# Optimization experiments

Measured on AMD Instinct MI355X. Metric: run time of the kernel, lower is better.

## Reference

```python
import jax, jax.numpy as jnp
import numpy as np

N = 100000      # nodes
E = 1600000     # edges
IN_DIM = 500
HID = 64
OUT = 40
BN_EPS = 1e-5


def setup_inputs() -> dict:
    key = jax.random.key(0)
    ks = jax.random.split(key, 20)
    x = jax.random.normal(ks[0], (N, IN_DIM), dtype=jnp.float32)
    edge_index = jax.random.randint(ks[1], (2, E), 0, N, dtype=jnp.int64)

    def lin(k, fin, fout):
        return jax.random.normal(k, (fin, fout), dtype=jnp.float32) / np.sqrt(fin).astype(np.float32)

    inp = {
        "x": x,
        "edge_index": edge_index,
        "W1": lin(ks[2], IN_DIM, HID),
        "b1": jnp.zeros((HID,), jnp.float32),
        "g1": jnp.ones((HID,), jnp.float32),
        "be1": jnp.zeros((HID,), jnp.float32),
        "m1": 0.1 * jax.random.normal(ks[3], (HID,), jnp.float32),
        "v1": jax.random.uniform(ks[4], (HID,), jnp.float32, 0.5, 1.5),
        "W2": lin(ks[5], HID, HID),
        "b2": jnp.zeros((HID,), jnp.float32),
        "g2": jnp.ones((HID,), jnp.float32),
        "be2": jnp.zeros((HID,), jnp.float32),
        "m2": 0.1 * jax.random.normal(ks[6], (HID,), jnp.float32),
        "v2": jax.random.uniform(ks[7], (HID,), jnp.float32, 0.5, 1.5),
        "W3": lin(ks[8], HID, OUT),
        "b3": jnp.zeros((OUT,), jnp.float32),
    }
    return inp


def _gcn_conv(h, src, dst, deg_inv_sqrt, W, b):
    # PyG GCNConv (add_self_loops=True, normalize=True, eval math):
    # out = D^-1/2 (A + I) D^-1/2 (h @ W) + b
    h = h @ W                                    # [N, F]
    norm = deg_inv_sqrt[src] * deg_inv_sqrt[dst]  # [E]
    msg = h[src] * norm[:, None]                  # [E, F] gather
    agg = jax.ops.segment_sum(msg, dst, num_segments=N)  # scatter-add
    agg = agg + h * (deg_inv_sqrt * deg_inv_sqrt)[:, None]  # self-loop term
    return agg + b


def reference(x, edge_index, W1, b1, g1, be1, m1, v1,
              W2, b2, g2, be2, m2, v2, W3, b3):
    src, dst = edge_index[0], edge_index[1]
    # degree including self-loop
    deg = jax.ops.segment_sum(jnp.ones((E,), x.dtype), dst, num_segments=N) + 1.0
    deg_inv_sqrt = jax.lax.rsqrt(deg)

    def bn(h, g, be, m, v):
        return (h - m) * jax.lax.rsqrt(v + BN_EPS) * g + be

    h = _gcn_conv(x, src, dst, deg_inv_sqrt, W1, b1)
    h = jax.nn.relu(bn(h, g1, be1, m1, v1))
    # dropout: identity in eval mode
    h = _gcn_conv(h, src, dst, deg_inv_sqrt, W2, b2)
    h = jax.nn.relu(bn(h, g2, be2, m2, v2))
    out = _gcn_conv(h, src, dst, deg_inv_sqrt, W3, b3)
    return jax.nn.log_softmax(out, axis=1)
```

## Files before the change

### kernel.cpp

```cpp
#include <hip/hip_runtime.h>
#include <math.h>

#define N_NODES 100000
#define N_EDGES 1600000
#define IN_DIM  500
#define HID     64
#define OUT_DIM 40
#define BN_EPS  1e-5f
#define SCAN_NB 98
#define NTILE   6250

typedef _Float16 f16;
typedef __attribute__((ext_vector_type(2))) _Float16 f16x2;
typedef __attribute__((ext_vector_type(8))) _Float16 f16x8;
typedef __attribute__((ext_vector_type(4))) float f32x4;

static inline int cdiv(long a, int b) { return (int)((a + b - 1) / b); }

__device__ inline unsigned short f2h_bits(float f) {
    f16 h = (f16)f;
    return __builtin_bit_cast(unsigned short, h);
}
__device__ inline f16x2 bits2h2(unsigned int u) {
    return __builtin_bit_cast(f16x2, u);
}

__global__ void k_count_deg(const int* __restrict__ ei, int* degi) {
    int e = blockIdx.x * 256 + threadIdx.x;
    if (e < N_EDGES) atomicAdd(&degi[ei[N_EDGES + e]], 1);
}

__global__ void k_scan1(const int* __restrict__ degi, int* __restrict__ rowptr,
                        int* __restrict__ blocksum, float* __restrict__ dis) {
    __shared__ int sd[256];
    int tid = threadIdx.x;
    int base = blockIdx.x * 1024 + tid * 4;
    int v0 = (base + 0 < N_NODES) ? degi[base + 0] : 0;
    int v1 = (base + 1 < N_NODES) ? degi[base + 1] : 0;
    int v2 = (base + 2 < N_NODES) ? degi[base + 2] : 0;
    int v3 = (base + 3 < N_NODES) ? degi[base + 3] : 0;
    if (base + 0 < N_NODES) dis[base + 0] = rsqrtf((float)v0 + 1.0f);
    if (base + 1 < N_NODES) dis[base + 1] = rsqrtf((float)v1 + 1.0f);
    if (base + 2 < N_NODES) dis[base + 2] = rsqrtf((float)v2 + 1.0f);
    if (base + 3 < N_NODES) dis[base + 3] = rsqrtf((float)v3 + 1.0f);
    int s = v0 + v1 + v2 + v3;
    sd[tid] = s;
    __syncthreads();
    for (int off = 1; off < 256; off <<= 1) {
        int t = (tid >= off) ? sd[tid - off] : 0;
        __syncthreads();
        sd[tid] += t;
        __syncthreads();
    }
    int excl = sd[tid] - s;
    if (base + 0 < N_NODES) rowptr[base + 0] = excl;
    if (base + 1 < N_NODES) rowptr[base + 1] = excl + v0;
    if (base + 2 < N_NODES) rowptr[base + 2] = excl + v0 + v1;
    if (base + 3 < N_NODES) rowptr[base + 3] = excl + v0 + v1 + v2;
    if (tid == 255) blocksum[blockIdx.x] = sd[255];
}

__global__ void k_scan2(int* __restrict__ blocksum, int* __restrict__ blockbase) {
    __shared__ int sd[128];
    int tid = threadIdx.x;
    int v = (tid < SCAN_NB) ? blocksum[tid] : 0;
    sd[tid] = v;
    __syncthreads();
    for (int off = 1; off < 128; off <<= 1) {
        int t = (tid >= off) ? sd[tid - off] : 0;
        __syncthreads();
        sd[tid] += t;
        __syncthreads();
    }
    if (tid < SCAN_NB) blockbase[tid] = sd[tid] - v;
}

__global__ void k_scan3(int* __restrict__ rowptr, const int* __restrict__ blockbase) {
    int add = blockbase[blockIdx.x];
    int base = blockIdx.x * 1024 + threadIdx.x * 4;
#pragma unroll
    for (int i = 0; i < 4; ++i)
        if (base + i < N_NODES) rowptr[base + i] += add;
}

__global__ void k_permute(const int* __restrict__ ei, const int* __restrict__ rowptr,
                          int* __restrict__ cursor, const float* __restrict__ dis,
                          uint2* __restrict__ epack) {
    int e = blockIdx.x * 256 + threadIdx.x;
    if (e >= N_EDGES) return;
    int s = ei[e];
    int d = ei[N_EDGES + e];
    int pos = rowptr[d] + atomicAdd(&cursor[d], 1);
    unsigned int hb = f2h_bits(dis[s] * dis[d]);
    epack[pos] = make_uint2((unsigned int)(s * 128), (hb << 16) | hb);
}

__device__ inline void convW_one(const float* W, unsigned short* wb,
                                 int idx, int K, int F) {
    int j    = idx & 7;
    int lane = (idx >> 3) & 63;
    int q    = idx >> 9;
    int t    = q >> 2, nt = q & 3;
    int n = nt * 16 + (lane & 15);
    int k = t * 32 + ((lane >> 4) << 3) + j;
    float v = (k < K && n < F) ? W[(long)k * F + n] : 0.f;
    wb[idx] = f2h_bits(v);
}

__global__ void k_convall(const float* __restrict__ W1, const float* __restrict__ W2,
                          const float* __restrict__ W3,
                          unsigned short* __restrict__ wb1,
                          unsigned short* __restrict__ wb2,
                          unsigned short* __restrict__ wb3) {
    int idx = blockIdx.x * 256 + threadIdx.x;
    if (idx < 32768) {
        convW_one(W1, wb1, idx, IN_DIM, HID);
    } else if (idx < 36864) {
        convW_one(W2, wb2, idx - 32768, HID, HID);
    } else {
        convW_one(W3, wb3, idx - 36864, HID, OUT_DIM);
    }
}

__global__ __launch_bounds__(256) void k_l1fused(
        const float* __restrict__ x,
        const unsigned short* __restrict__ wb,
        unsigned short* __restrict__ h) {
    __shared__ unsigned short l[16 * 520];
    const int rt = blockIdx.x;
    const int tid = threadIdx.x;

#pragma unroll
    for (int it = 0; it < 8; ++it) {
        int slot = it * 256 + tid;
        int row = slot >> 7, kq = slot & 127;
        float4 v = make_float4(0.f, 0.f, 0.f, 0.f);
        if (kq < 125)
            v = *reinterpret_cast<const float4*>(x + ((long)rt * 16 + row) * IN_DIM + kq * 4);
        unsigned int u0 = (unsigned int)f2h_bits(v.x) | ((unsigned int)f2h_bits(v.y) << 16);
        unsigned int u1 = (unsigned int)f2h_bits(v.z) | ((unsigned int)f2h_bits(v.w) << 16);
        *reinterpret_cast<uint2*>(&l[row * 520 + kq * 4]) = make_uint2(u0, u1);
    }
    __syncthreads();

    const int wid  = tid >> 6;
    const int lane = tid & 63;
    const int l15  = lane & 15;
    const int lhi  = lane >> 4;

    const f16x8* bp = reinterpret_cast<const f16x8*>(wb) + wid * 64 + lane;
    const unsigned short* arow = &l[l15 * 520 + lhi * 8];

    f32x4 acc = (f32x4){0.f, 0.f, 0.f, 0.f};
    f16x8 ca = *reinterpret_cast<const f16x8*>(arow);
    f16x8 cb = bp[0];

#pragma unroll
    for (int t = 0; t < 16; ++t) {
        f16x8 na, nb;
        if (t < 15) {
            na = *reinterpret_cast<const f16x8*>(arow + (t + 1) * 32);
            nb = bp[(t + 1) * 256];
        }
        acc = __builtin_amdgcn_mfma_f32_16x16x32_f16(ca, cb, acc, 0, 0, 0);
        if (t < 15) { ca = na; cb = nb; }
    }

#pragma unroll
    for (int rr = 0; rr < 4; ++rr) {
        long grow = (long)rt * 16 + lhi * 4 + rr;
        h[grow * 64 + wid * 16 + l15] = f2h_bits(acc[rr]);
    }
}

template <int T>
__global__ __launch_bounds__(256) void k_gemm_packed(
        const unsigned short* __restrict__ xp,
        const unsigned short* __restrict__ wb,
        unsigned short* __restrict__ h) {
    const int tid  = threadIdx.x;
    const int wid  = tid >> 6;
    const int lane = tid & 63;
    const int rt   = blockIdx.x * 4 + wid;
    if (rt >= NTILE) return;

    const f16x8* ap = reinterpret_cast<const f16x8*>(xp) + (long)rt * T * 64 + lane;
    const f16x8* bp = reinterpret_cast<const f16x8*>(wb) + lane;

    f32x4 acc[4];
#pragma unroll
    for (int nt = 0; nt < 4; ++nt) acc[nt] = (f32x4){0.f, 0.f, 0.f, 0.f};

    f16x8 ca = ap[0];
    f16x8 cb0 = bp[0], cb1 = bp[64], cb2 = bp[128], cb3 = bp[192];

    for (int t = 0; t < T; ++t) {
        f16x8 na, nb0, nb1, nb2, nb3;
        if (t + 1 < T) {
            na  = ap[(t + 1) * 64];
            nb0 = bp[((t + 1) * 4 + 0) * 64];
            nb1 = bp[((t + 1) * 4 + 1) * 64];
            nb2 = bp[((t + 1) * 4 + 2) * 64];
            nb3 = bp[((t + 1) * 4 + 3) * 64];
        }
        acc[0] = __builtin_amdgcn_mfma_f32_16x16x32_f16(ca, cb0, acc[0], 0, 0, 0);
        acc[1] = __builtin_amdgcn_mfma_f32_16x16x32_f16(ca, cb1, acc[1], 0, 0, 0);
        acc[2] = __builtin_amdgcn_mfma_f32_16x16x32_f16(ca, cb2, acc[2], 0, 0, 0);
        acc[3] = __builtin_amdgcn_mfma_f32_16x16x32_f16(ca, cb3, acc[3], 0, 0, 0);
        if (t + 1 < T) { ca = na; cb0 = nb0; cb1 = nb1; cb2 = nb2; cb3 = nb3; }
    }

    const int l15 = lane & 15, lhi = lane >> 4;
#pragma unroll
    for (int nt = 0; nt < 4; ++nt) {
        int coln = nt * 16 + l15;
#pragma unroll
        for (int rr = 0; rr < 4; ++rr) {
            long grow = (long)rt * 16 + lhi * 4 + rr;
            h[grow * 64 + coln] = f2h_bits(acc[nt][rr]);
        }
    }
}

__global__ __launch_bounds__(256) void k_agg_bn_relu(
        const unsigned short* __restrict__ h, const int* __restrict__ rowptr,
        const int* __restrict__ degi, const uint2* __restrict__ epack,
        const float* __restrict__ dis,
        const float* __restrict__ bias, const float* __restrict__ g,
        const float* __restrict__ be, const float* __restrict__ m,
        const float* __restrict__ v, unsigned short* __restrict__ xp_out) {
    int node = blockIdx.x * 4 + (threadIdx.x >> 6);
    if (node >= N_NODES) return;
    const int lane = threadIdx.x & 63;
    const int e8 = lane >> 3, c8 = lane & 7;

    const int start = rowptr[node];
    const int cnt   = degi[node];
    const uint2* ep = epack + start;
    const char*  hb = (const char*)h + c8 * 16;

    f16x2 a[4] = {(f16x2)0, (f16x2)0, (f16x2)0, (f16x2)0};

    auto batch = [&](int j) {
        int jj = j + e8;
        bool valid = jj < cnt;
        uint2 mv = ep[valid ? jj : 0];
        f16x2 w2 = bits2h2(valid ? mv.y : 0u);
        uint4 hv = *(const uint4*)(hb + mv.x);
        a[0] += bits2h2(hv.x) * w2;
        a[1] += bits2h2(hv.y) * w2;
        a[2] += bits2h2(hv.z) * w2;
        a[3] += bits2h2(hv.w) * w2;
    };

    int j = 0;
    for (; j + 8 < cnt; j += 16) { batch(j); batch(j + 8); }
    if (j < cnt) batch(j);

#pragma unroll
    for (int off = 8; off < 64; off <<= 1) {
#pragma unroll
        for (int i = 0; i < 4; ++i) {
            unsigned int u = __builtin_bit_cast(unsigned int, a[i]);
            a[i] += bits2h2((unsigned int)__shfl_xor((int)u, off));
        }
    }

    if (e8 == 0) {
        float d = dis[node], d2 = d * d;
        uint4 sv = *(const uint4*)((const char*)h + (long)node * 128 + c8 * 16);
        f16x2 s01 = bits2h2(sv.x), s23 = bits2h2(sv.y);
        f16x2 s45 = bits2h2(sv.z), s67 = bits2h2(sv.w);
        float av[8] = {(float)a[0][0], (float)a[0][1], (float)a[1][0], (float)a[1][1],
                       (float)a[2][0], (float)a[2][1], (float)a[3][0], (float)a[3][1]};
        float sf[8] = {(float)s01[0], (float)s01[1], (float)s23[0], (float)s23[1],
                       (float)s45[0], (float)s45[1], (float)s67[0], (float)s67[1]};
        float4 bb0 = *(const float4*)(bias + c8 * 8), bb1 = *(const float4*)(bias + c8 * 8 + 4);
        float4 mm0 = *(const float4*)(m + c8 * 8),    mm1 = *(const float4*)(m + c8 * 8 + 4);
        float4 vv0 = *(const float4*)(v + c8 * 8),    vv1 = *(const float4*)(v + c8 * 8 + 4);
        float4 gg0 = *(const float4*)(g + c8 * 8),    gg1 = *(const float4*)(g + c8 * 8 + 4);
        float4 ee0 = *(const float4*)(be + c8 * 8),   ee1 = *(const float4*)(be + c8 * 8 + 4);
        float bbv[8] = {bb0.x, bb0.y, bb0.z, bb0.w, bb1.x, bb1.y, bb1.z, bb1.w};
        float mmv[8] = {mm0.x, mm0.y, mm0.z, mm0.w, mm1.x, mm1.y, mm1.z, mm1.w};
        float vvv[8] = {vv0.x, vv0.y, vv0.z, vv0.w, vv1.x, vv1.y, vv1.z, vv1.w};
        float ggv[8] = {gg0.x, gg0.y, gg0.z, gg0.w, gg1.x, gg1.y, gg1.z, gg1.w};
        float eev[8] = {ee0.x, ee0.y, ee0.z, ee0.w, ee1.x, ee1.y, ee1.z, ee1.w};

        unsigned int u[4];
#pragma unroll
        for (int p = 0; p < 4; ++p) {
            float r0 = av[2 * p]     + sf[2 * p]     * d2 + bbv[2 * p];
            float r1 = av[2 * p + 1] + sf[2 * p + 1] * d2 + bbv[2 * p + 1];
            r0 = fmaxf((r0 - mmv[2 * p])     * rsqrtf(vvv[2 * p]     + BN_EPS) * ggv[2 * p]     + eev[2 * p],     0.f);
            r1 = fmaxf((r1 - mmv[2 * p + 1]) * rsqrtf(vvv[2 * p + 1] + BN_EPS) * ggv[2 * p + 1] + eev[2 * p + 1], 0.f);
            u[p] = (unsigned int)f2h_bits(r0) | ((unsigned int)f2h_bits(r1) << 16);
        }

        int n16 = node & 15, rt2 = node >> 4;
        long base = (((long)rt2 * 2 + (c8 >> 2)) * 64 + (c8 & 3) * 16 + n16) * 8;
        *reinterpret_cast<uint4*>(xp_out + base) = make_uint4(u[0], u[1], u[2], u[3]);
    }
}

__global__ __launch_bounds__(256) void k_agg_lsm(
        const unsigned short* __restrict__ h, const int* __restrict__ rowptr,
        const int* __restrict__ degi, const uint2* __restrict__ epack,
        const float* __restrict__ dis,
        const float* __restrict__ bias, float* __restrict__ out) {
    int node = blockIdx.x * 4 + (threadIdx.x >> 6);
    if (node >= N_NODES) return;
    const int lane = threadIdx.x & 63;
    const int e8 = lane >> 3, c8 = lane & 7;

    const int start = rowptr[node];
    const int cnt   = degi[node];
    const uint2* ep = epack + start;
    const char*  hb = (const char*)h + c8 * 16;

    f16x2 a[4] = {(f16x2)0, (f16x2)0, (f16x2)0, (f16x2)0};

    auto batch = [&](int j) {
        int jj = j + e8;
        bool valid = jj < cnt;
        uint2 mv = ep[valid ? jj : 0];
        f16x2 w2 = bits2h2(valid ? mv.y : 0u);
        uint4 hv = *(const uint4*)(hb + mv.x);
        a[0] += bits2h2(hv.x) * w2;
        a[1] += bits2h2(hv.y) * w2;
        a[2] += bits2h2(hv.z) * w2;
        a[3] += bits2h2(hv.w) * w2;
    };

    int j = 0;
    for (; j + 8 < cnt; j += 16) { batch(j); batch(j + 8); }
    if (j < cnt) batch(j);

#pragma unroll
    for (int off = 8; off < 64; off <<= 1) {
#pragma unroll
        for (int i = 0; i < 4; ++i) {
            unsigned int u = __builtin_bit_cast(unsigned int, a[i]);
            a[i] += bits2h2((unsigned int)__shfl_xor((int)u, off));
        }
    }

    const bool ok = c8 < 5;
    float d = dis[node], d2 = d * d;
    uint4 sv = *(const uint4*)((const char*)h + (long)node * 128 + c8 * 16);
    f16x2 s01 = bits2h2(sv.x), s23 = bits2h2(sv.y);
    f16x2 s45 = bits2h2(sv.z), s67 = bits2h2(sv.w);
    float av[8] = {(float)a[0][0], (float)a[0][1], (float)a[1][0], (float)a[1][1],
                   (float)a[2][0], (float)a[2][1], (float)a[3][0], (float)a[3][1]};
    float sf[8] = {(float)s01[0], (float)s01[1], (float)s23[0], (float)s23[1],
                   (float)s45[0], (float)s45[1], (float)s67[0], (float)s67[1]};
    float vals[8];
    float mx = -INFINITY;
    if (ok) {
        float4 bb0 = *(const float4*)(bias + c8 * 8), bb1 = *(const float4*)(bias + c8 * 8 + 4);
        float bbv[8] = {bb0.x, bb0.y, bb0.z, bb0.w, bb1.x, bb1.y, bb1.z, bb1.w};
#pragma unroll
        for (int i = 0; i < 8; ++i) {
            vals[i] = av[i] + sf[i] * d2 + bbv[i];
            mx = fmaxf(mx, vals[i]);
        }
    }
#pragma unroll
    for (int o = 1; o < 8; o <<= 1) mx = fmaxf(mx, __shfl_xor(mx, o));
    float es = 0.f;
    if (ok) {
#pragma unroll
        for (int i = 0; i < 8; ++i) es += expf(vals[i] - mx);
    }
#pragma unroll
    for (int o = 1; o < 8; o <<= 1) es += __shfl_xor(es, o);
    float ls = logf(es);

    if (e8 == 0 && ok) {
        float* op = out + (long)node * 40 + c8 * 8;
        *(float4*)op = make_float4(vals[0] - mx - ls, vals[1] - mx - ls,
                                   vals[2] - mx - ls, vals[3] - mx - ls);
        *(float4*)(op + 4) = make_float4(vals[4] - mx - ls, vals[5] - mx - ls,
                                         vals[6] - mx - ls, vals[7] - mx - ls);
    }
}

extern "C" void kernel_launch(void* const* d_in, const int* in_sizes, int n_in,
                              void* d_out, int out_size, void* d_ws, size_t ws_size,
                              hipStream_t stream) {
    const float* x   = (const float*)d_in[0];
    const int*   ei  = (const int*)d_in[1];
    const float* W1  = (const float*)d_in[2];
    const float* b1  = (const float*)d_in[3];
    const float* g1  = (const float*)d_in[4];
    const float* be1 = (const float*)d_in[5];
    const float* m1  = (const float*)d_in[6];
    const float* v1  = (const float*)d_in[7];
    const float* W2  = (const float*)d_in[8];
    const float* b2  = (const float*)d_in[9];
    const float* g2  = (const float*)d_in[10];
    const float* be2 = (const float*)d_in[11];
    const float* m2  = (const float*)d_in[12];
    const float* v2  = (const float*)d_in[13];
    const float* W3  = (const float*)d_in[14];
    const float* b3  = (const float*)d_in[15];
    float* out = (float*)d_out;

    float* ws        = (float*)d_ws;
    float* dis       = ws;
    int*   degi      = (int*)(ws + 100096);
    int*   cursor    = (int*)(ws + 200192);
    int*   rowptr    = (int*)(ws + 300288);
    int*   blocksum  = (int*)(ws + 400384);
    int*   blockbase = (int*)(ws + 400512);
    uint2* epack     = (uint2*)(ws + 400640);
    unsigned short* bufH = (unsigned short*)(ws + 3600640);
    unsigned short* xp2  = (unsigned short*)(ws + 32400640);
    unsigned short* xp3  = (unsigned short*)(ws + 35600640);
    unsigned short* wb1  = (unsigned short*)(ws + 38800640);
    unsigned short* wb2  = (unsigned short*)(ws + 38817024);
    unsigned short* wb3  = (unsigned short*)(ws + 38819072);

    hipMemsetAsync(degi, 0, 2 * 100096 * sizeof(int), stream);
    k_count_deg<<<cdiv(N_EDGES, 256), 256, 0, stream>>>(ei, degi);
    k_scan1<<<SCAN_NB, 256, 0, stream>>>(degi, rowptr, blocksum, dis);
    k_scan2<<<1, 128, 0, stream>>>(blocksum, blockbase);
    k_scan3<<<SCAN_NB, 256, 0, stream>>>(rowptr, blockbase);
    k_permute<<<cdiv(N_EDGES, 256), 256, 0, stream>>>(ei, rowptr, cursor, dis, epack);

    k_convall<<<160, 256, 0, stream>>>(W1, W2, W3, wb1, wb2, wb3);

    const int gemm_grid = cdiv(NTILE, 4);
    const int agg_grid  = cdiv(N_NODES, 4);

    k_l1fused<<<NTILE, 256, 0, stream>>>(x, wb1, bufH);
    k_agg_bn_relu<<<agg_grid, 256, 0, stream>>>(bufH, rowptr, degi, epack,
                                                dis, b1, g1, be1, m1, v1, xp2);

    k_gemm_packed<2><<<gemm_grid, 256, 0, stream>>>(xp2, wb2, bufH);
    k_agg_bn_relu<<<agg_grid, 256, 0, stream>>>(bufH, rowptr, degi, epack,
                                                dis, b2, g2, be2, m2, v2, xp3);

    k_gemm_packed<2><<<gemm_grid, 256, 0, stream>>>(xp3, wb3, bufH);
    k_agg_lsm<<<agg_grid, 256, 0, stream>>>(bufH, rowptr, degi, epack,
                                            dis, b3, out);
}
```

Measured before the change: 394.5 us.

## Fold self-loops into CSR edges and precompute fused BN scale/shift in fp16

Self-loop terms become explicit CSR entries: the scan counts degree+1 per node, and scan3 writes each node's self edge with weight 1/deg at the start of its row and sets cursor to 1. The aggregation kernels then drop the separate self-feature load and the dis/degi lookups, taking the count from rowptr differences. Bias and eval BatchNorm are folded into a per-channel fp16 scale and shift computed once, so the epilogue is a packed fp16 FMA plus ReLU. This adds one gathered edge per node and does the BN math in fp16, so rounding error may rise.

```diff
diff --git a/kernel.cpp b/kernel.cpp
--- a/kernel.cpp
+++ b/kernel.cpp
@@ -35,15 +35,16 @@
     __shared__ int sd[256];
     int tid = threadIdx.x;
     int base = blockIdx.x * 1024 + tid * 4;
-    int v0 = (base + 0 < N_NODES) ? degi[base + 0] : 0;
-    int v1 = (base + 1 < N_NODES) ? degi[base + 1] : 0;
-    int v2 = (base + 2 < N_NODES) ? degi[base + 2] : 0;
-    int v3 = (base + 3 < N_NODES) ? degi[base + 3] : 0;
+    int v0 = (base + 0 < N_NODES) ? degi[base + 0] : -1;
+    int v1 = (base + 1 < N_NODES) ? degi[base + 1] : -1;
+    int v2 = (base + 2 < N_NODES) ? degi[base + 2] : -1;
+    int v3 = (base + 3 < N_NODES) ? degi[base + 3] : -1;
     if (base + 0 < N_NODES) dis[base + 0] = rsqrtf((float)v0 + 1.0f);
     if (base + 1 < N_NODES) dis[base + 1] = rsqrtf((float)v1 + 1.0f);
     if (base + 2 < N_NODES) dis[base + 2] = rsqrtf((float)v2 + 1.0f);
     if (base + 3 < N_NODES) dis[base + 3] = rsqrtf((float)v3 + 1.0f);
-    int s = v0 + v1 + v2 + v3;
+    int w0 = v0 + 1, w1 = v1 + 1, w2 = v2 + 1, w3 = v3 + 1;
+    int s = w0 + w1 + w2 + w3;
     sd[tid] = s;
     __syncthreads();
     for (int off = 1; off < 256; off <<= 1) {
@@ -54,9 +55,9 @@
     }
     int excl = sd[tid] - s;
     if (base + 0 < N_NODES) rowptr[base + 0] = excl;
-    if (base + 1 < N_NODES) rowptr[base + 1] = excl + v0;
-    if (base + 2 < N_NODES) rowptr[base + 2] = excl + v0 + v1;
-    if (base + 3 < N_NODES) rowptr[base + 3] = excl + v0 + v1 + v2;
+    if (base + 1 < N_NODES) rowptr[base + 1] = excl + w0;
+    if (base + 2 < N_NODES) rowptr[base + 2] = excl + w0 + w1;
+    if (base + 3 < N_NODES) rowptr[base + 3] = excl + w0 + w1 + w2;
     if (tid == 255) blocksum[blockIdx.x] = sd[255];
 }
 
@@ -75,12 +76,25 @@
     if (tid < SCAN_NB) blockbase[tid] = sd[tid] - v;
 }
 
-__global__ void k_scan3(int* __restrict__ rowptr, const int* __restrict__ blockbase) {
+__global__ void k_scan3(int* __restrict__ rowptr, const int* __restrict__ blockbase,
+                        const int* __restrict__ degi, int* __restrict__ cursor,
+                        uint2* __restrict__ epack) {
     int add = blockbase[blockIdx.x];
     int base = blockIdx.x * 1024 + threadIdx.x * 4;
 #pragma unroll
-    for (int i = 0; i < 4; ++i)
-        if (base + i < N_NODES) rowptr[base + i] += add;
+    for (int i = 0; i < 4; ++i) {
+        int node = base + i;
+        if (node < N_NODES) {
+            int rp = rowptr[node] + add;
+            rowptr[node] = rp;
+            float d2 = 1.0f / (float)(degi[node] + 1);
+            unsigned int hb = f2h_bits(d2);
+            epack[rp] = make_uint2((unsigned int)(node * 128), (hb << 16) | hb);
+            cursor[node] = 1;
+        }
+    }
+    if (blockIdx.x == 0 && threadIdx.x == 0)
+        rowptr[N_NODES] = N_EDGES + N_NODES;
 }
 
 __global__ void k_permute(const int* __restrict__ ei, const int* __restrict__ rowptr,
@@ -122,6 +136,26 @@
     }
 }
 
+__global__ void k_bnfold(const float* __restrict__ b1, const float* __restrict__ g1,
+                         const float* __restrict__ be1, const float* __restrict__ m1,
+                         const float* __restrict__ v1,
+                         const float* __restrict__ b2, const float* __restrict__ g2,
+                         const float* __restrict__ be2, const float* __restrict__ m2,
+                         const float* __restrict__ v2,
+                         unsigned short* __restrict__ sc1,
+                         unsigned short* __restrict__ sc2) {
+    int t = threadIdx.x;
+    int c = t & 63;
+    const float *b, *g, *be, *m, *v;
+    unsigned short* sc;
+    if (t < 64) { b = b1; g = g1; be = be1; m = m1; v = v1; sc = sc1; }
+    else        { b = b2; g = g2; be = be2; m = m2; v = v2; sc = sc2; }
+    float S = g[c] * rsqrtf(v[c] + BN_EPS);
+    float C = (b[c] - m[c]) * S + be[c];
+    sc[c]      = f2h_bits(S);
+    sc[64 + c] = f2h_bits(C);
+}
+
 __global__ __launch_bounds__(256) void k_l1fused(
         const float* __restrict__ x,
         const unsigned short* __restrict__ wb,
@@ -224,18 +258,15 @@
 
 __global__ __launch_bounds__(256) void k_agg_bn_relu(
         const unsigned short* __restrict__ h, const int* __restrict__ rowptr,
-        const int* __restrict__ degi, const uint2* __restrict__ epack,
-        const float* __restrict__ dis,
-        const float* __restrict__ bias, const float* __restrict__ g,
-        const float* __restrict__ be, const float* __restrict__ m,
-        const float* __restrict__ v, unsigned short* __restrict__ xp_out) {
+        const uint2* __restrict__ epack, const unsigned short* __restrict__ sc,
+        unsigned short* __restrict__ xp_out) {
     int node = blockIdx.x * 4 + (threadIdx.x >> 6);
     if (node >= N_NODES) return;
     const int lane = threadIdx.x & 63;
     const int e8 = lane >> 3, c8 = lane & 7;
 
     const int start = rowptr[node];
-    const int cnt   = degi[node];
+    const int cnt   = rowptr[node + 1] - start;
     const uint2* ep = epack + start;
     const char*  hb = (const char*)h + c8 * 16;
 
@@ -267,33 +298,17 @@
     }
 
     if (e8 == 0) {
-        float d = dis[node], d2 = d * d;
-        uint4 sv = *(const uint4*)((const char*)h + (long)node * 128 + c8 * 16);
-        f16x2 s01 = bits2h2(sv.x), s23 = bits2h2(sv.y);
-        f16x2 s45 = bits2h2(sv.z), s67 = bits2h2(sv.w);
-        float av[8] = {(float)a[0][0], (float)a[0][1], (float)a[1][0], (float)a[1][1],
-                       (float)a[2][0], (float)a[2][1], (float)a[3][0], (float)a[3][1]};
-        float sf[8] = {(float)s01[0], (float)s01[1], (float)s23[0], (float)s23[1],
-                       (float)s45[0], (float)s45[1], (float)s67[0], (float)s67[1]};
-        float4 bb0 = *(const float4*)(bias + c8 * 8), bb1 = *(const float4*)(bias + c8 * 8 + 4);
-        float4 mm0 = *(const float4*)(m + c8 * 8),    mm1 = *(const float4*)(m + c8 * 8 + 4);
-        float4 vv0 = *(const float4*)(v + c8 * 8),    vv1 = *(const float4*)(v + c8 * 8 + 4);
-        float4 gg0 = *(const float4*)(g + c8 * 8),    gg1 = *(const float4*)(g + c8 * 8 + 4);
-        float4 ee0 = *(const float4*)(be + c8 * 8),   ee1 = *(const float4*)(be + c8 * 8 + 4);
-        float bbv[8] = {bb0.x, bb0.y, bb0.z, bb0.w, bb1.x, bb1.y, bb1.z, bb1.w};
-        float mmv[8] = {mm0.x, mm0.y, mm0.z, mm0.w, mm1.x, mm1.y, mm1.z, mm1.w};
-        float vvv[8] = {vv0.x, vv0.y, vv0.z, vv0.w, vv1.x, vv1.y, vv1.z, vv1.w};
-        float ggv[8] = {gg0.x, gg0.y, gg0.z, gg0.w, gg1.x, gg1.y, gg1.z, gg1.w};
-        float eev[8] = {ee0.x, ee0.y, ee0.z, ee0.w, ee1.x, ee1.y, ee1.z, ee1.w};
-
+        uint4 Su = *(const uint4*)(sc + c8 * 8);
+        uint4 Cu = *(const uint4*)(sc + 64 + c8 * 8);
+        unsigned int sw[4] = {Su.x, Su.y, Su.z, Su.w};
+        unsigned int cw[4] = {Cu.x, Cu.y, Cu.z, Cu.w};
         unsigned int u[4];
 #pragma unroll
         for (int p = 0; p < 4; ++p) {
-            float r0 = av[2 * p]     + sf[2 * p]     * d2 + bbv[2 * p];
-            float r1 = av[2 * p + 1] + sf[2 * p + 1] * d2 + bbv[2 * p + 1];
-            r0 = fmaxf((r0 - mmv[2 * p])     * rsqrtf(vvv[2 * p]     + BN_EPS) * ggv[2 * p]     + eev[2 * p],     0.f);
-            r1 = fmaxf((r1 - mmv[2 * p + 1]) * rsqrtf(vvv[2 * p + 1] + BN_EPS) * ggv[2 * p + 1] + eev[2 * p + 1], 0.f);
-            u[p] = (unsigned int)f2h_bits(r0) | ((unsigned int)f2h_bits(r1) << 16);
+            f16x2 r = a[p] * bits2h2(sw[p]) + bits2h2(cw[p]);
+            r[0] = r[0] > (f16)0 ? r[0] : (f16)0;
+            r[1] = r[1] > (f16)0 ? r[1] : (f16)0;
+            u[p] = __builtin_bit_cast(unsigned int, r);
         }
 
         int n16 = node & 15, rt2 = node >> 4;
@@ -304,8 +319,7 @@
 
 __global__ __launch_bounds__(256) void k_agg_lsm(
         const unsigned short* __restrict__ h, const int* __restrict__ rowptr,
-        const int* __restrict__ degi, const uint2* __restrict__ epack,
-        const float* __restrict__ dis,
+        const uint2* __restrict__ epack,
         const float* __restrict__ bias, float* __restrict__ out) {
     int node = blockIdx.x * 4 + (threadIdx.x >> 6);
     if (node >= N_NODES) return;
@@ -313,7 +327,7 @@
     const int e8 = lane >> 3, c8 = lane & 7;
 
     const int start = rowptr[node];
-    const int cnt   = degi[node];
+    const int cnt   = rowptr[node + 1] - start;
     const uint2* ep = epack + start;
     const char*  hb = (const char*)h + c8 * 16;
 
@@ -345,14 +359,8 @@
     }
 
     const bool ok = c8 < 5;
-    float d = dis[node], d2 = d * d;
-    uint4 sv = *(const uint4*)((const char*)h + (long)node * 128 + c8 * 16);
-    f16x2 s01 = bits2h2(sv.x), s23 = bits2h2(sv.y);
-    f16x2 s45 = bits2h2(sv.z), s67 = bits2h2(sv.w);
     float av[8] = {(float)a[0][0], (float)a[0][1], (float)a[1][0], (float)a[1][1],
                    (float)a[2][0], (float)a[2][1], (float)a[3][0], (float)a[3][1]};
-    float sf[8] = {(float)s01[0], (float)s01[1], (float)s23[0], (float)s23[1],
-                   (float)s45[0], (float)s45[1], (float)s67[0], (float)s67[1]};
     float vals[8];
     float mx = -INFINITY;
     if (ok) {
@@ -360,7 +368,7 @@
         float bbv[8] = {bb0.x, bb0.y, bb0.z, bb0.w, bb1.x, bb1.y, bb1.z, bb1.w};
 #pragma unroll
         for (int i = 0; i < 8; ++i) {
-            vals[i] = av[i] + sf[i] * d2 + bbv[i];
+            vals[i] = av[i] + bbv[i];
             mx = fmaxf(mx, vals[i]);
         }
     }
@@ -413,34 +421,34 @@
     int*   blocksum  = (int*)(ws + 400384);
     int*   blockbase = (int*)(ws + 400512);
     uint2* epack     = (uint2*)(ws + 400640);
-    unsigned short* bufH = (unsigned short*)(ws + 3600640);
+    unsigned short* bufH = (unsigned short*)(ws + 3800640);
     unsigned short* xp2  = (unsigned short*)(ws + 32400640);
     unsigned short* xp3  = (unsigned short*)(ws + 35600640);
     unsigned short* wb1  = (unsigned short*)(ws + 38800640);
     unsigned short* wb2  = (unsigned short*)(ws + 38817024);
     unsigned short* wb3  = (unsigned short*)(ws + 38819072);
-
-    hipMemsetAsync(degi, 0, 2 * 100096 * sizeof(int), stream);
+    unsigned short* sc1  = (unsigned short*)(ws + 38821120);
+    unsigned short* sc2  = sc1 + 128;
+
+    hipMemsetAsync(degi, 0, 100096 * sizeof(int), stream);
     k_count_deg<<<cdiv(N_EDGES, 256), 256, 0, stream>>>(ei, degi);
     k_scan1<<<SCAN_NB, 256, 0, stream>>>(degi, rowptr, blocksum, dis);
     k_scan2<<<1, 128, 0, stream>>>(blocksum, blockbase);
-    k_scan3<<<SCAN_NB, 256, 0, stream>>>(rowptr, blockbase);
+    k_scan3<<<SCAN_NB, 256, 0, stream>>>(rowptr, blockbase, degi, cursor, epack);
     k_permute<<<cdiv(N_EDGES, 256), 256, 0, stream>>>(ei, rowptr, cursor, dis, epack);
 
     k_convall<<<160, 256, 0, stream>>>(W1, W2, W3, wb1, wb2, wb3);
+    k_bnfold<<<1, 128, 0, stream>>>(b1, g1, be1, m1, v1, b2, g2, be2, m2, v2, sc1, sc2);
 
     const int gemm_grid = cdiv(NTILE, 4);
     const int agg_grid  = cdiv(N_NODES, 4);
 
     k_l1fused<<<NTILE, 256, 0, stream>>>(x, wb1, bufH);
-    k_agg_bn_relu<<<agg_grid, 256, 0, stream>>>(bufH, rowptr, degi, epack,
-                                                dis, b1, g1, be1, m1, v1, xp2);
+    k_agg_bn_relu<<<agg_grid, 256, 0, stream>>>(bufH, rowptr, epack, sc1, xp2);
 
     k_gemm_packed<2><<<gemm_grid, 256, 0, stream>>>(xp2, wb2, bufH);
-    k_agg_bn_relu<<<agg_grid, 256, 0, stream>>>(bufH, rowptr, degi, epack,
-                                                dis, b2, g2, be2, m2, v2, xp3);
+    k_agg_bn_relu<<<agg_grid, 256, 0, stream>>>(bufH, rowptr, epack, sc2, xp3);
 
     k_gemm_packed<2><<<gemm_grid, 256, 0, stream>>>(xp3, wb3, bufH);
-    k_agg_lsm<<<agg_grid, 256, 0, stream>>>(bufH, rowptr, degi, epack,
-                                            dis, b3, out);
-}
+    k_agg_lsm<<<agg_grid, 256, 0, stream>>>(bufH, rowptr, epack, b3, out);
+}
```

New measurement: 363.1 us. 1.09x faster.
